# Kernel optimization log

Measured on AMD Instinct MI355X. Metric: run time of the kernel, lower is better.

## Reference

```python
import jax, jax.numpy as jnp
import numpy as np

GROUP_SIZE = 128


def dequantize_int4(packed, scales, group_size=GROUP_SIZE, dtype=jnp.float16):
    # packed: [O, I//2] bytes; low nibble -> even cols, high nibble -> odd cols
    O = packed.shape[0]
    I = packed.shape[1] * 2
    low = (packed & 15).astype(jnp.int8) - 8
    high = ((packed >> 4) & 15).astype(jnp.int8) - 8
    unpacked = jnp.stack([low, high], axis=-1).reshape(O, I)  # interleave low/high
    G = I // group_size
    grouped = unpacked.reshape(O, G, group_size).astype(jnp.float32)
    deq = grouped * scales.astype(jnp.float32)[:, :, None]  # per-group scale
    return deq.reshape(O, I).astype(dtype)


def setup_inputs() -> dict:
    key = jax.random.key(0)
    k1, k2, k3 = jax.random.split(key, 3)
    B, S, IN, OUT = 4, 2048, 4096, 11008
    G = IN // GROUP_SIZE
    x = jax.random.normal(k1, (B, S, IN), dtype=jnp.float16)
    packed = jax.random.randint(k2, (OUT, IN // 2), 0, 256, dtype=jnp.int32)
    scales = (jax.random.uniform(k3, (OUT, G), dtype=jnp.float32) * 0.05 + 0.001).astype(jnp.float16)
    return {"x": x, "packed": packed, "scales": scales}


def reference(x, packed, scales):
    x = x.astype(jnp.float16)
    W = dequantize_int4(packed, scales)  # [OUT, IN] fp16
    # nn.functional.linear: x @ W^T
    return jnp.einsum('bsi,oi->bso', x, W)
```

## Files before the change

### kernel.cpp

```cpp
#include <hip/hip_runtime.h>

#define M_DIM 8192
#define N_DIM 11008
#define K_DIM 4096
#define GROUPS 32
#define WQROW 512
#define LDSK 72

typedef short s16x8 __attribute__((ext_vector_type(8)));
typedef _Float16 f16x8 __attribute__((ext_vector_type(8)));
typedef _Float16 h2 __attribute__((ext_vector_type(2)));
typedef float f32x4 __attribute__((ext_vector_type(4)));
typedef unsigned short u16;
typedef unsigned int u32;

union f32u { float f; unsigned u; };
union h16u { u16 u; _Float16 h; };

__device__ __forceinline__ u16 f2bf(float f) {
  f32u v; v.f = f;
  unsigned r = v.u + 0x7FFFu + ((v.u >> 16) & 1u);
  return (u16)(r >> 16);
}
__device__ __forceinline__ float bf2f(u16 b) {
  f32u v; v.u = ((unsigned)b) << 16; return v.f;
}
__device__ __forceinline__ float h2f(u16 b) {
  h16u v; v.u = b; return (float)v.h;
}

__global__ void probe_mode_kernel(const void* __restrict__ scales,
                                  int* __restrict__ mode_out) {
  __shared__ int cnt[3];
  int t = threadIdx.x;
  if (t < 3) cnt[t] = 0;
  __syncthreads();
  float f0 = ((const float*)scales)[t];
  u16  hu  = ((const u16*)scales)[t];
  float f1 = h2f(hu);
  float f2 = bf2f(hu);
  if (f0 > 0.0004f && f0 < 0.065f) atomicAdd(&cnt[0], 1);
  if (f1 > 0.0004f && f1 < 0.065f) atomicAdd(&cnt[1], 1);
  if (f2 > 0.0004f && f2 < 0.065f) atomicAdd(&cnt[2], 1);
  __syncthreads();
  if (t == 0) {
    int m;
    if      (cnt[1] >= 240) m = 1;
    else if (cnt[2] >= 240) m = 2;
    else                    m = 0;
    mode_out[0] = m;
  }
}

__global__ __launch_bounds__(256) void convert_x_nat_kernel(
    const float* __restrict__ xf, u16* __restrict__ xh,
    const int* __restrict__ modep) {
  if (modep && modep[0] != 0) return;
  const int total8 = M_DIM * (K_DIM / 8);
  int idx = blockIdx.x * 256 + threadIdx.x;
  const int stride = gridDim.x * 256;
  for (; idx < total8; idx += stride) {
    const float4* p = (const float4*)(xf + (size_t)idx * 8);
    float4 a = p[0], b = p[1];
    union { _Float16 h[8]; s16x8 v; } r;
    r.h[0] = (_Float16)a.x; r.h[1] = (_Float16)a.y;
    r.h[2] = (_Float16)a.z; r.h[3] = (_Float16)a.w;
    r.h[4] = (_Float16)b.x; r.h[5] = (_Float16)b.y;
    r.h[6] = (_Float16)b.z; r.h[7] = (_Float16)b.w;
    *(s16x8*)(xh + (size_t)idx * 8) = r.v;
  }
}

__global__ __launch_bounds__(256) void dequant_w_kernel(
    const int* __restrict__ packed, const float* __restrict__ scf,
    u16* __restrict__ wf, const int* __restrict__ modep) {
  if (modep && modep[0] != 0) return;
  const int total = N_DIM * (K_DIM / 8);
  int idx = blockIdx.x * 256 + threadIdx.x;
  const int stride = gridDim.x * 256;
  for (; idx < total; idx += stride) {
    const int col = idx >> 9;
    const int d   = idx & 511;
    const float s = scf[col * GROUPS + (d >> 4)];
    const int4 p  = ((const int4*)packed)[idx];
    const int vals[4] = {p.x, p.y, p.z, p.w};
    union { _Float16 h[8]; s16x8 v; } r;
    #pragma unroll
    for (int e = 0; e < 4; ++e) {
      int b = vals[e] & 255;
      r.h[2 * e]     = (_Float16)((float)((b & 15) - 8) * s);
      r.h[2 * e + 1] = (_Float16)((float)(((b >> 4) & 15) - 8) * s);
    }
    *(s16x8*)(wf + (size_t)idx * 8) = r.v;
  }
}

__global__ __launch_bounds__(256, 2) void q4gemm_big_kernel(
    const u16* __restrict__ xh,
    const u16* __restrict__ wf,
    float* __restrict__ out,
    const int* __restrict__ modep)
{
  if (modep && modep[0] != 0) return;

  __shared__ _Float16 As[3][128 * 64];

  const int tid  = threadIdx.x;
  const int lane = tid & 63;
  const int wv   = tid >> 6;
  const int wn   = wv * 64;
  const int ln15 = lane & 15;
  const int lk   = lane >> 4;

  int bid = blockIdx.x;
  int f   = (bid & 7) * 344 + (bid >> 3);
  int bn  = f / 64;
  int bm  = f - bn * 64;
  const int m0 = bm * 128;
  const int n0 = bn * 256;

  const u16* abase[4];
  #pragma unroll
  for (int q = 0; q < 4; ++q) {
    int row = q * 32 + wv * 8 + (lane >> 3);
    abase[q] = xh + (size_t)(m0 + row) * K_DIM + (((lane & 7) ^ (lane >> 3)) * 8);
  }

#define STAGE(PB, T) do { \
    _Float16* dst = &As[(PB)][0]; \
    _Pragma("unroll") \
    for (int q = 0; q < 4; ++q) \
      __builtin_amdgcn_global_load_lds( \
          (const __attribute__((address_space(1))) void*)(abase[q] + (T) * 64), \
          (__attribute__((address_space(3))) void*)(dst + q * 2048 + wv * 512), \
          16, 0, 0); \
  } while (0)

  const u16* pB[4];
  #pragma unroll
  for (int j = 0; j < 4; ++j) {
    int col = n0 + wn + j * 16 + ln15;
    pB[j] = wf + (size_t)col * K_DIM + lk * 8;
  }

#define LOADB(RB, T) do { \
    _Pragma("unroll") \
    for (int j = 0; j < 4; ++j) { \
      RB[j]     = *(const f16x8*)(pB[j] + (T) * 64); \
      RB[j + 4] = *(const f16x8*)(pB[j] + (T) * 64 + 32); \
    } \
  } while (0)

#define COMPUTE(RB, PB) do { \
    const _Float16* asb = &As[(PB)][0]; \
    _Pragma("unroll") \
    for (int kkc = 0; kkc < 2; ++kkc) { \
      _Pragma("unroll") \
      for (int i = 0; i < 8; ++i) { \
        const int row  = i * 16 + ln15; \
        const int slot = (kkc * 4 + lk) ^ (ln15 & 7); \
        f16x8 af = *(const f16x8*)&asb[row * 64 + slot * 8]; \
        acc[i][0] = __builtin_amdgcn_mfma_f32_16x16x32_f16(af, RB[kkc * 4 + 0], acc[i][0], 0, 0, 0); \
        acc[i][1] = __builtin_amdgcn_mfma_f32_16x16x32_f16(af, RB[kkc * 4 + 1], acc[i][1], 0, 0, 0); \
        acc[i][2] = __builtin_amdgcn_mfma_f32_16x16x32_f16(af, RB[kkc * 4 + 2], acc[i][2], 0, 0, 0); \
        acc[i][3] = __builtin_amdgcn_mfma_f32_16x16x32_f16(af, RB[kkc * 4 + 3], acc[i][3], 0, 0, 0); \
      } \
    } \
  } while (0)

  f32x4 acc[8][4];
  #pragma unroll
  for (int i = 0; i < 8; ++i)
    #pragma unroll
    for (int j = 0; j < 4; ++j)
      acc[i][j] = f32x4{0.f, 0.f, 0.f, 0.f};

  f16x8 rbE[8], rbO[8];

  STAGE(0, 0);
  STAGE(1, 1);
  LOADB(rbE, 0);
  LOADB(rbO, 1);
  asm volatile("s_waitcnt vmcnt(0)" ::: "memory");

  int p0 = 0, p1 = 1, p2 = 2;

  for (int tp = 0; tp < 32; ++tp) {
    const int t0 = 2 * tp;
    const int t1 = t0 + 1;

    asm volatile("s_waitcnt vmcnt(12)" ::: "memory");
    __builtin_amdgcn_s_barrier();
    __builtin_amdgcn_sched_barrier(0);

    if (t0 + 2 < 64) STAGE(p2, t0 + 2);

    __builtin_amdgcn_s_setprio(1);
    COMPUTE(rbE, p0);
    __builtin_amdgcn_s_setprio(0);

    if (t0 + 2 < 64) LOADB(rbE, t0 + 2);

    if (tp == 31) {
      asm volatile("s_waitcnt vmcnt(0)" ::: "memory");
    } else {
      asm volatile("s_waitcnt vmcnt(12)" ::: "memory");
    }
    __builtin_amdgcn_s_barrier();
    __builtin_amdgcn_sched_barrier(0);

    if (t1 + 2 < 64) STAGE(p0, t1 + 2);

    __builtin_amdgcn_s_setprio(1);
    COMPUTE(rbO, p1);
    __builtin_amdgcn_s_setprio(0);

    if (t1 + 2 < 64) LOADB(rbO, t1 + 2);

    int tmp = p2; p2 = p1; p1 = p0; p0 = tmp;
  }

  #pragma unroll
  for (int i = 0; i < 8; ++i) {
    int r0 = m0 + i * 16 + (lane >> 4) * 4;
    #pragma unroll
    for (int j = 0; j < 4; ++j) {
      int cc = n0 + wn + j * 16 + ln15;
      #pragma unroll
      for (int r = 0; r < 4; ++r)
        out[(size_t)(r0 + r) * N_DIM + cc] = acc[i][j][r];
    }
  }
#undef STAGE
#undef LOADB
#undef COMPUTE
}

__global__ __launch_bounds__(256) void convert_x_perm_kernel(
    const float* __restrict__ xf, u16* __restrict__ xh,
    const int* __restrict__ modep) {
  if (modep && modep[0] != 0) return;
  const int total8 = M_DIM * (K_DIM / 8);
  int idx = blockIdx.x * 256 + threadIdx.x;
  const int stride = gridDim.x * 256;
  for (; idx < total8; idx += stride) {
    const float4* p = (const float4*)(xf + (size_t)idx * 8);
    float4 a = p[0], b = p[1];
    union { _Float16 h[8]; s16x8 v; } r;
    r.h[0] = (_Float16)a.x; r.h[1] = (_Float16)b.x;
    r.h[2] = (_Float16)a.y; r.h[3] = (_Float16)b.y;
    r.h[4] = (_Float16)a.z; r.h[5] = (_Float16)b.z;
    r.h[6] = (_Float16)a.w; r.h[7] = (_Float16)b.w;
    *(s16x8*)(xh + (size_t)idx * 8) = r.v;
  }
}

__global__ __launch_bounds__(256) void repack_w_kernel(
    const int* __restrict__ packed, u32* __restrict__ wq) {
  const int total = N_DIM * WQROW;
  int idx = blockIdx.x * 256 + threadIdx.x;
  const int stride = gridDim.x * 256;
  for (; idx < total; idx += stride) {
    const int4 p = ((const int4*)packed)[idx];
    wq[idx] = (u32)(p.x & 255) | ((u32)(p.y & 255) << 8) |
              ((u32)(p.z & 255) << 16) | ((u32)p.w << 24);
  }
}

__device__ __forceinline__ f16x8 dq8(u32 q, h2 s2) {
  const u32 M = 0x000F000Fu, G = 0x64006400u;
  const h2 bias = {(_Float16)(-1032.0f), (_Float16)(-1032.0f)};
  union { u32 u; h2 h; } a0, a1, a2, a3;
  a0.u = (q & M) | G;
  a1.u = ((q >> 4) & M) | G;
  a2.u = ((q >> 8) & M) | G;
  a3.u = ((q >> 12) & M) | G;
  a0.h = (a0.h + bias) * s2;
  a1.h = (a1.h + bias) * s2;
  a2.h = (a2.h + bias) * s2;
  a3.h = (a3.h + bias) * s2;
  union { u32 u[4]; f16x8 f; } r;
  r.u[0] = a0.u; r.u[1] = a1.u; r.u[2] = a2.u; r.u[3] = a3.u;
  return r.f;
}

__global__ __launch_bounds__(256, 2) void q4gemm_mid_kernel(
    const u16* __restrict__ xh, const u32* __restrict__ wq,
    const float* __restrict__ scf, float* __restrict__ out,
    const int* __restrict__ modep)
{
  if (modep && modep[0] != 0) return;

  __shared__ _Float16 As[3][128 * 64];

  const int tid  = threadIdx.x;
  const int lane = tid & 63;
  const int wv   = tid >> 6;
  const int wn   = wv * 64;
  const int ln15 = lane & 15;
  const int lk   = lane >> 4;

  int bid = blockIdx.x;
  int f   = (bid & 7) * 344 + (bid >> 3);
  int bn  = f / 64;
  int bm  = f - bn * 64;
  const int m0 = bm * 128;
  const int n0 = bn * 256;

  const u16* abase[4];
  #pragma unroll
  for (int q = 0; q < 4; ++q) {
    int row = q * 32 + wv * 8 + (lane >> 3);
    abase[q] = xh + (size_t)(m0 + row) * K_DIM + (((lane & 7) ^ (lane >> 3)) * 8);
  }

#define STAGE(PB, T) do { \
    _Float16* dst = &As[(PB)][0]; \
    _Pragma("unroll") \
    for (int q = 0; q < 4; ++q) \
      __builtin_amdgcn_global_load_lds( \
          (const __attribute__((address_space(1))) void*)(abase[q] + (T) * 64), \
          (__attribute__((address_space(3))) void*)(dst + q * 2048 + wv * 512), \
          16, 0, 0); \
  } while (0)

#define LOADB(RB, T) do { \
    _Pragma("unroll") \
    for (int j = 0; j < 4; ++j) { \
      RB[j]     = wq[pcol[j] + (T) * 8]; \
      RB[j + 4] = wq[pcol[j] + (T) * 8 + 4]; \
    } \
  } while (0)

#define COMPUTE(RB, PB) do { \
    const _Float16* asb = &As[(PB)][0]; \
    _Pragma("unroll") \
    for (int kkc = 0; kkc < 2; ++kkc) { \
      f16x8 bfr0 = dq8(RB[kkc * 4 + 0], s2[0]); \
      f16x8 bfr1 = dq8(RB[kkc * 4 + 1], s2[1]); \
      f16x8 bfr2 = dq8(RB[kkc * 4 + 2], s2[2]); \
      f16x8 bfr3 = dq8(RB[kkc * 4 + 3], s2[3]); \
      _Pragma("unroll") \
      for (int i = 0; i < 8; ++i) { \
        const int row  = i * 16 + ln15; \
        const int slot = (kkc * 4 + lk) ^ (ln15 & 7); \
        f16x8 af = *(const f16x8*)&asb[row * 64 + slot * 8]; \
        acc[i][0] = __builtin_amdgcn_mfma_f32_16x16x32_f16(af, bfr0, acc[i][0], 0, 0, 0); \
        acc[i][1] = __builtin_amdgcn_mfma_f32_16x16x32_f16(af, bfr1, acc[i][1], 0, 0, 0); \
        acc[i][2] = __builtin_amdgcn_mfma_f32_16x16x32_f16(af, bfr2, acc[i][2], 0, 0, 0); \
        acc[i][3] = __builtin_amdgcn_mfma_f32_16x16x32_f16(af, bfr3, acc[i][3], 0, 0, 0); \
      } \
    } \
  } while (0)

  int pcol[4], scol[4];
  #pragma unroll
  for (int j = 0; j < 4; ++j) {
    int col = n0 + wn + j * 16 + ln15;
    pcol[j] = col * WQROW + lk;
    scol[j] = col * GROUPS;
  }

  f32x4 acc[8][4];
  #pragma unroll
  for (int i = 0; i < 8; ++i)
    #pragma unroll
    for (int j = 0; j < 4; ++j)
      acc[i][j] = f32x4{0.f, 0.f, 0.f, 0.f};

  u32 rbE[8], rbO[8];
  float snextf[4];
  h2 s2[4];

  STAGE(0, 0);
  STAGE(1, 1);
  LOADB(rbE, 0);
  LOADB(rbO, 1);
  #pragma unroll
  for (int j = 0; j < 4; ++j) snextf[j] = scf[scol[j]];
  asm volatile("s_waitcnt vmcnt(0)" ::: "memory");

  int p0 = 0, p1 = 1, p2 = 2;

  for (int tp = 0; tp < 32; ++tp) {
    const int t0 = 2 * tp;
    const int t1 = t0 + 1;

    asm volatile("s_waitcnt vmcnt(12)" ::: "memory");
    __builtin_amdgcn_s_barrier();
    __builtin_amdgcn_sched_barrier(0);

    #pragma unroll
    for (int j = 0; j < 4; ++j) {
      _Float16 sh = (_Float16)snextf[j];
      s2[j] = h2{sh, sh};
    }
    if (t0 + 2 < 64) STAGE(p2, t0 + 2);

    __builtin_amdgcn_s_setprio(1);
    COMPUTE(rbE, p0);
    __builtin_amdgcn_s_setprio(0);

    if (t0 + 2 < 64) LOADB(rbE, t0 + 2);
    {
      const int gn = (tp + 1 > 31) ? 31 : (tp + 1);
      #pragma unroll
      for (int j = 0; j < 4; ++j) snextf[j] = scf[scol[j] + gn];
    }

    if (tp == 31) {
      asm volatile("s_waitcnt vmcnt(0)" ::: "memory");
    } else {
      asm volatile("s_waitcnt vmcnt(12)" ::: "memory");
    }
    __builtin_amdgcn_s_barrier();
    __builtin_amdgcn_sched_barrier(0);

    if (t1 + 2 < 64) STAGE(p0, t1 + 2);

    __builtin_amdgcn_s_setprio(1);
    COMPUTE(rbO, p1);
    __builtin_amdgcn_s_setprio(0);

    if (t1 + 2 < 64) LOADB(rbO, t1 + 2);

    int tmp = p2; p2 = p1; p1 = p0; p0 = tmp;
  }

  #pragma unroll
  for (int i = 0; i < 8; ++i) {
    int r0 = m0 + i * 16 + (lane >> 4) * 4;
    #pragma unroll
    for (int j = 0; j < 4; ++j) {
      int cc = n0 + wn + j * 16 + ln15;
      #pragma unroll
      for (int r = 0; r < 4; ++r)
        out[(size_t)(r0 + r) * N_DIM + cc] = acc[i][j][r];
    }
  }
#undef STAGE
#undef LOADB
#undef COMPUTE
}

__global__ __launch_bounds__(256) void q4gemm_slow_kernel(
    const void* __restrict__ xraw,
    const int*  __restrict__ packed,
    const void* __restrict__ scraw,
    float* __restrict__ out,
    const int* __restrict__ modep,
    int skip0)
{
  const int mode = modep ? modep[0] : 0;
  if (skip0 && mode == 0) return;

  __shared__ u16 Asl[128 * LDSK];
  __shared__ u16 Bsl[128 * LDSK];

  const int tid  = threadIdx.x;
  const int lane = tid & 63;
  const int wv   = tid >> 6;
  const int wm   = (wv >> 1) * 64;
  const int wn   = (wv & 1) * 64;
  const int n0   = blockIdx.x * 128;
  const int m0   = blockIdx.y * 128;

  f32x4 acc[4][4];
  #pragma unroll
  for (int i = 0; i < 4; ++i)
    #pragma unroll
    for (int j = 0; j < 4; ++j)
      acc[i][j] = f32x4{0.f, 0.f, 0.f, 0.f};

  const int lrow16 = lane & 15;
  const int lk8    = (lane >> 4) * 8;

  for (int k0 = 0; k0 < K_DIM; k0 += 64) {
    if (mode == 0) {
      const float* xf = (const float*)xraw;
      #pragma unroll
      for (int it = 0; it < 4; ++it) {
        int s = tid + it * 256;
        int row = s >> 3, c8 = (s & 7) * 8;
        const float4* p = (const float4*)(xf + (size_t)(m0 + row) * K_DIM + k0 + c8);
        float4 v0 = p[0], v1 = p[1];
        u16 tmp[8] = { f2bf(v0.x), f2bf(v0.y), f2bf(v0.z), f2bf(v0.w),
                       f2bf(v1.x), f2bf(v1.y), f2bf(v1.z), f2bf(v1.w) };
        *(s16x8*)&Asl[row * LDSK + c8] = *(const s16x8*)tmp;
      }
    } else if (mode == 1) {
      const u16* xhh = (const u16*)xraw;
      #pragma unroll
      for (int it = 0; it < 4; ++it) {
        int s = tid + it * 256;
        int row = s >> 3, c8 = (s & 7) * 8;
        s16x8 v = *(const s16x8*)(xhh + (size_t)(m0 + row) * K_DIM + k0 + c8);
        u16 tmp[8];
        #pragma unroll
        for (int j = 0; j < 8; ++j) tmp[j] = f2bf(h2f((u16)v[j]));
        *(s16x8*)&Asl[row * LDSK + c8] = *(const s16x8*)tmp;
      }
    } else {
      const u16* xhh = (const u16*)xraw;
      #pragma unroll
      for (int it = 0; it < 4; ++it) {
        int s = tid + it * 256;
        int row = s >> 3, c8 = (s & 7) * 8;
        s16x8 v = *(const s16x8*)(xhh + (size_t)(m0 + row) * K_DIM + k0 + c8);
        *(s16x8*)&Asl[row * LDSK + c8] = v;
      }
    }

    {
      int row  = tid >> 1;
      int half = tid & 1;
      int srw  = n0 + row;
      int g    = k0 >> 7;
      float scale;
      if      (mode == 0) scale = ((const float*)scraw)[(size_t)srw * GROUPS + g];
      else if (mode == 1) scale = h2f(((const u16*)scraw)[(size_t)srw * GROUPS + g]);
      else                scale = bf2f(((const u16*)scraw)[(size_t)srw * GROUPS + g]);

      const int4* pp = (const int4*)(packed + (size_t)srw * (K_DIM / 2) + (k0 >> 1) + half * 16);
      #pragma unroll
      for (int j = 0; j < 4; ++j) {
        int4 pv = pp[j];
        int vals[4] = {pv.x, pv.y, pv.z, pv.w};
        u16 w[8];
        #pragma unroll
        for (int e = 0; e < 4; ++e) {
          int b = vals[e] & 255;
          w[e * 2]     = f2bf(scale * (float)((b & 15) - 8));
          w[e * 2 + 1] = f2bf(scale * (float)(((b >> 4) & 15) - 8));
        }
        int i0 = half * 16 + j * 4;
        *(s16x8*)&Bsl[row * LDSK + i0 * 2] = *(const s16x8*)w;
      }
    }
    __syncthreads();

    #pragma unroll
    for (int kk = 0; kk < 64; kk += 32) {
      s16x8 af[4], bfr[4];
      int klane = kk + lk8;
      #pragma unroll
      for (int i = 0; i < 4; ++i)
        af[i] = *(const s16x8*)&Asl[(wm + i * 16 + lrow16) * LDSK + klane];
      #pragma unroll
      for (int i = 0; i < 4; ++i)
        bfr[i] = *(const s16x8*)&Bsl[(wn + i * 16 + lrow16) * LDSK + klane];
      #pragma unroll
      for (int i = 0; i < 4; ++i)
        #pragma unroll
        for (int j = 0; j < 4; ++j)
          acc[i][j] = __builtin_amdgcn_mfma_f32_16x16x32_bf16(af[i], bfr[j], acc[i][j], 0, 0, 0);
    }
    __syncthreads();
  }

  #pragma unroll
  for (int i = 0; i < 4; ++i) {
    int rbase = m0 + wm + i * 16 + ((lane >> 4) * 4);
    #pragma unroll
    for (int j = 0; j < 4; ++j) {
      int c = n0 + wn + j * 16 + (lane & 15);
      #pragma unroll
      for (int r = 0; r < 4; ++r)
        out[(size_t)(rbase + r) * N_DIM + c] = acc[i][j][r];
    }
  }
}

extern "C" void kernel_launch(void* const* d_in, const int* in_sizes, int n_in,
                              void* d_out, int out_size, void* d_ws, size_t ws_size,
                              hipStream_t stream) {
  const void* x      = d_in[0];
  const int*  packed = (const int*)d_in[1];
  const void* scales = d_in[2];
  float* out = (float*)d_out;

  const size_t XB = (size_t)M_DIM * K_DIM * 2;
  const size_t WF = (size_t)N_DIM * K_DIM * 2;
  const size_t WQ = (size_t)N_DIM * WQROW * 4;
  const size_t NEED_BIG = 256 + XB + WF;
  const size_t NEED_MID = 256 + XB + WQ;

  int* mode_flag = nullptr;
  if (ws_size >= 4) {
    mode_flag = (int*)d_ws;
    probe_mode_kernel<<<dim3(1), dim3(256), 0, stream>>>(scales, mode_flag);
  }

  int fast = 0;
  if (mode_flag && ws_size >= NEED_BIG) fast = 2;
  else if (mode_flag && ws_size >= NEED_MID) fast = 1;

  if (fast == 2) {
    u16* xh = (u16*)((char*)d_ws + 256);
    u16* wf = (u16*)((char*)d_ws + 256 + XB);
    convert_x_nat_kernel<<<dim3(2048), dim3(256), 0, stream>>>(
        (const float*)x, xh, mode_flag);
    dequant_w_kernel<<<dim3(2048), dim3(256), 0, stream>>>(
        packed, (const float*)scales, wf, mode_flag);
    q4gemm_big_kernel<<<dim3(2752), dim3(256), 0, stream>>>(
        xh, wf, out, mode_flag);
  } else if (fast == 1) {
    u16* xh = (u16*)((char*)d_ws + 256);
    u32* wq = (u32*)((char*)d_ws + 256 + XB);
    convert_x_perm_kernel<<<dim3(2048), dim3(256), 0, stream>>>(
        (const float*)x, xh, mode_flag);
    repack_w_kernel<<<dim3(2048), dim3(256), 0, stream>>>(packed, wq);
    q4gemm_mid_kernel<<<dim3(2752), dim3(256), 0, stream>>>(
        xh, wq, (const float*)scales, out, mode_flag);
  }

  q4gemm_slow_kernel<<<dim3(N_DIM / 128, M_DIM / 128), dim3(256), 0, stream>>>(
      x, packed, scales, out, mode_flag, fast);
}
```

Before: 924.6 us.

## Restructure GEMM main loop to four-buffer LDS ring with one barrier per pair

Grows the A-tile LDS ring from three to four buffers and stages two K-tiles at a time, so the main loop needs one barrier per pair of K-steps instead of two. Fewer barriers should cut synchronisation stalls and let more loads be in flight across compute. LDS use rises from 48KB to 64KB per block, which may hurt the two-blocks-per-CU occupancy target, and the B register prefetch now re-loads tile 63 redundantly at the tail. Output writes also become nontemporal stores to avoid polluting the cache.

```diff
diff --git a/kernel.cpp b/kernel.cpp
--- a/kernel.cpp
+++ b/kernel.cpp
@@ -103,7 +103,7 @@
 {
   if (modep && modep[0] != 0) return;
 
-  __shared__ _Float16 As[3][128 * 64];
+  __shared__ _Float16 As[4][128 * 64];
 
   const int tid  = threadIdx.x;
   const int lane = tid & 63;
@@ -179,45 +179,41 @@
 
   STAGE(0, 0);
   STAGE(1, 1);
+  STAGE(2, 2);
+  STAGE(3, 3);
   LOADB(rbE, 0);
   LOADB(rbO, 1);
   asm volatile("s_waitcnt vmcnt(0)" ::: "memory");
-
-  int p0 = 0, p1 = 1, p2 = 2;
-
-  for (int tp = 0; tp < 32; ++tp) {
-    const int t0 = 2 * tp;
-    const int t1 = t0 + 1;
-
-    asm volatile("s_waitcnt vmcnt(12)" ::: "memory");
-    __builtin_amdgcn_s_barrier();
-    __builtin_amdgcn_sched_barrier(0);
-
-    if (t0 + 2 < 64) STAGE(p2, t0 + 2);
+  __builtin_amdgcn_s_barrier();
+
+  #pragma unroll 1
+  for (int P = 0; P < 32; ++P) {
+    const int b0 = (P & 1) * 2;
+    const int s0 = b0 ^ 2;
+
+    if (P > 0) {
+      asm volatile("s_waitcnt vmcnt(16)" ::: "memory");
+      __builtin_amdgcn_s_barrier();
+      __builtin_amdgcn_sched_barrier(0);
+      if (P <= 30) {
+        STAGE(s0, 2 * P + 2);
+        STAGE(s0 + 1, 2 * P + 3);
+      }
+      __builtin_amdgcn_sched_barrier(0);
+    }
+
+    const int tE = (2 * P + 2 > 63) ? 63 : (2 * P + 2);
+    const int tO = (2 * P + 3 > 63) ? 63 : (2 * P + 3);
 
     __builtin_amdgcn_s_setprio(1);
-    COMPUTE(rbE, p0);
+    COMPUTE(rbE, b0);
     __builtin_amdgcn_s_setprio(0);
-
-    if (t0 + 2 < 64) LOADB(rbE, t0 + 2);
-
-    if (tp == 31) {
-      asm volatile("s_waitcnt vmcnt(0)" ::: "memory");
-    } else {
-      asm volatile("s_waitcnt vmcnt(12)" ::: "memory");
-    }
-    __builtin_amdgcn_s_barrier();
-    __builtin_amdgcn_sched_barrier(0);
-
-    if (t1 + 2 < 64) STAGE(p0, t1 + 2);
+    LOADB(rbE, tE);
 
     __builtin_amdgcn_s_setprio(1);
-    COMPUTE(rbO, p1);
+    COMPUTE(rbO, b0 + 1);
     __builtin_amdgcn_s_setprio(0);
-
-    if (t1 + 2 < 64) LOADB(rbO, t1 + 2);
-
-    int tmp = p2; p2 = p1; p1 = p0; p0 = tmp;
+    LOADB(rbO, tO);
   }
 
   #pragma unroll
@@ -228,7 +224,7 @@
       int cc = n0 + wn + j * 16 + ln15;
       #pragma unroll
       for (int r = 0; r < 4; ++r)
-        out[(size_t)(r0 + r) * N_DIM + cc] = acc[i][j][r];
+        __builtin_nontemporal_store(acc[i][j][r], &out[(size_t)(r0 + r) * N_DIM + cc]);
     }
   }
 #undef STAGE
```

Measured after the change: 905.6 us. -2.1%, faster.
